# Kernel optimization log

Hardware: AMD Instinct MI355X
Metric: run time of the kernel (lower is better)

The kernel has to match this reference:

```python
import jax, jax.numpy as jnp
import numpy as np

B, M, C = 32, 64, 36
INPUT_DIM, HIDDEN, N_CLASS = 1024, 512, 1000
NEG_INF = -1e10


def setup_inputs() -> dict:
    key = jax.random.key(0)
    ks = jax.random.split(key, 16)
    s = 0.02
    return {
        "mention_embeddings": jax.random.normal(ks[0], (B, M, INPUT_DIM), jnp.float32),
        "class_labels": jax.random.uniform(ks[1], (B, C, N_CLASS), jnp.float32),
        "mention_mask": jnp.ones((B, M), jnp.float32),
        "class_mask": jnp.ones((B, C), jnp.float32),
        # visual_embedder: Linear(n_class, H) -> ReLU -> Linear(H, H)
        "vw1": jax.random.normal(ks[2], (N_CLASS, HIDDEN), jnp.float32) * s,
        "vb1": jnp.zeros((HIDDEN,), jnp.float32),
        "vw2": jax.random.normal(ks[3], (HIDDEN, HIDDEN), jnp.float32) * s,
        "vb2": jnp.zeros((HIDDEN,), jnp.float32),
        # mention_embedder: Linear(input_dim, H) -> ReLU -> Linear(H, H)
        "mw1": jax.random.normal(ks[4], (INPUT_DIM, HIDDEN), jnp.float32) * s,
        "mb1": jnp.zeros((HIDDEN,), jnp.float32),
        "mw2": jax.random.normal(ks[5], (HIDDEN, HIDDEN), jnp.float32) * s,
        "mb2": jnp.zeros((HIDDEN,), jnp.float32),
        # attention: Linear(H, H) -> ReLU -> Linear(H, 1)
        "aw1": jax.random.normal(ks[6], (HIDDEN, HIDDEN), jnp.float32) * s,
        "ab1": jnp.zeros((HIDDEN,), jnp.float32),
        "aw2": jax.random.normal(ks[7], (HIDDEN, 1), jnp.float32) * s,
        "ab2": jnp.zeros((1,), jnp.float32),
    }


def reference(mention_embeddings, class_labels, mention_mask, class_mask,
              vw1, vb1, vw2, vb2, mw1, mb1, mw2, mb2, aw1, ab1, aw2, ab2):
    # visual embeddings: (B, C, H)
    vis = jax.nn.relu(class_labels @ vw1 + vb1) @ vw2 + vb2
    # mention embeddings: (B, M, H)
    men = jax.nn.relu(mention_embeddings @ mw1 + mb1) @ mw2 + mb2
    # broadcast outer product: (B, M, C, H)
    prod = men[:, :, None, :] * vis[:, None, :, :]
    # 2-layer MLP attention score -> (B, M, C)
    h = jax.nn.relu(prod @ aw1 + ab1)
    attn = (h @ aw2 + ab2)[..., 0]
    # masking
    attn = attn * mention_mask[:, :, None] * class_mask[:, None, :]
    attn = jnp.where(attn != 0, attn, NEG_INF)
    return attn
```

## Files before the change

### kernel.cpp

```cpp
#include <hip/hip_runtime.h>

typedef _Float16 f16;
typedef _Float16 f16x8 __attribute__((ext_vector_type(8)));
typedef _Float16 f16x4 __attribute__((ext_vector_type(4)));
typedef float f32x4 __attribute__((ext_vector_type(4)));
typedef float fl4 __attribute__((ext_vector_type(4)));

#define NEG_INF_F (-1e10f)

__device__ __forceinline__ void stage16(const f16* g, f16* l) {
    __builtin_amdgcn_global_load_lds((const __attribute__((address_space(1))) void*)g,
                                     (__attribute__((address_space(3))) void*)l, 16, 0, 0);
}

__global__ __launch_bounds__(256) void prep2(const float* __restrict__ me,
                                             const float* __restrict__ mw1,
                                             const float* __restrict__ vw1,
                                             const float* __restrict__ mw2,
                                             const float* __restrict__ vw2,
                                             const float* __restrict__ aw1,
                                             const float* __restrict__ cl,
                                             f16* __restrict__ me_h,
                                             f16* __restrict__ mw1t, f16* __restrict__ vw1t,
                                             f16* __restrict__ mw2t, f16* __restrict__ vw2t,
                                             f16* __restrict__ aw1t, f16* __restrict__ cl_h) {
    int bx = blockIdx.x, t = threadIdx.x;
    if (bx < 1792) {
        __shared__ float tile[32][33];
        const float* src; f16* dst; int Ksrc, Kp, tid;
        if (bx < 512)       { src = mw1; dst = mw1t; Ksrc = 1024; Kp = 1024; tid = bx; }
        else if (bx < 1024) { src = vw1; dst = vw1t; Ksrc = 1000; Kp = 1024; tid = bx - 512; }
        else if (bx < 1280) { src = mw2; dst = mw2t; Ksrc = 512;  Kp = 512;  tid = bx - 1024; }
        else if (bx < 1536) { src = vw2; dst = vw2t; Ksrc = 512;  Kp = 512;  tid = bx - 1280; }
        else                { src = aw1; dst = aw1t; Ksrc = 512;  Kp = 512;  tid = bx - 1536; }
        int tk = tid >> 4, tn = tid & 15;
        int x = t & 31, y = t >> 5;
        #pragma unroll
        for (int r = 0; r < 4; r++) {
            int k = tk * 32 + y * 4 + r;
            tile[y * 4 + r][x] = (k < Ksrc) ? src[k * 512 + tn * 32 + x] : 0.f;
        }
        __syncthreads();
        #pragma unroll
        for (int r = 0; r < 4; r++) {
            int n = tn * 32 + y * 4 + r;
            dst[n * Kp + tk * 32 + x] = (f16)tile[x][y * 4 + r];
        }
        return;
    }
    if (bx < 3840) {
        int i = (bx - 1792) * 256 + t;
        fl4 v = *(const fl4*)(me + i * 4);
        f16x4 h;
        #pragma unroll
        for (int e = 0; e < 4; e++) h[e] = (f16)v[e];
        *(f16x4*)(me_h + i * 4) = h;
        return;
    }
    {
        int i = (bx - 3840) * 256 + t;
        int idx = i * 4;
        int r = idx >> 10, k0 = idx & 1023;
        f16x4 h;
        if (k0 < 1000) {
            fl4 v = *(const fl4*)(cl + r * 1000 + k0);
            #pragma unroll
            for (int e = 0; e < 4; e++) h[e] = (f16)v[e];
        } else {
            #pragma unroll
            for (int e = 0; e < 4; e++) h[e] = (f16)0.f;
        }
        *(f16x4*)(cl_h + idx) = h;
    }
}

__global__ __launch_bounds__(256, 4) void gemm_stg2(const f16* __restrict__ Am,
                                                    const f16* __restrict__ Av,
                                                    const f16* __restrict__ Wm,
                                                    const f16* __restrict__ Wv,
                                                    const float* __restrict__ bm,
                                                    const float* __restrict__ bv,
                                                    f16* __restrict__ om,
                                                    f16* __restrict__ ov,
                                                    int K, int relu) {
    __shared__ f16 ab[2][2048], bb[2][2048];

    int t = threadIdx.x, lane = t & 63, w = t >> 6;
    int rl = lane & 15, kg = lane >> 4;
    int mq = w & 1, nq = w >> 1;
    bool isv = blockIdx.x >= 32;
    int mb = isv ? blockIdx.x - 32 : blockIdx.x;
    const f16* A = isv ? Av : Am;
    const f16* Wt = isv ? Wv : Wm;
    const float* bias = isv ? bv : bm;
    f16* out = isv ? ov : om;
    int m0 = mb * 64, n0 = blockIdx.y * 64;
    int pu = kg ^ ((rl >> 1) & 3);

    int srow = t >> 2;
    int sk8 = (t & 3) ^ ((srow >> 1) & 3);
    const f16* a_src = A + (m0 + srow) * K + sk8 * 8;
    const f16* b_src = Wt + (n0 + srow) * K + sk8 * 8;
    int nsteps = K >> 5;

    f32x4 acc[2][2] = {};

    stage16(a_src, &ab[0][t * 8]);
    stage16(b_src, &bb[0][t * 8]);
    __syncthreads();

    for (int s = 0; s < nsteps; s++) {
        int cur = s & 1;
        if (s + 1 < nsteps) {
            int k1 = (s + 1) * 32;
            stage16(a_src + k1, &ab[cur ^ 1][t * 8]);
            stage16(b_src + k1, &bb[cur ^ 1][t * 8]);
        }
        f16x8 af[2], bf[2];
        #pragma unroll
        for (int f = 0; f < 2; f++) {
            af[f] = *(const f16x8*)&ab[cur][((mq * 32 + f * 16 + rl) * 4 + pu) * 8];
            bf[f] = *(const f16x8*)&bb[cur][((nq * 32 + f * 16 + rl) * 4 + pu) * 8];
        }
        #pragma unroll
        for (int fi = 0; fi < 2; fi++)
            #pragma unroll
            for (int fj = 0; fj < 2; fj++)
                acc[fi][fj] = __builtin_amdgcn_mfma_f32_16x16x32_f16(af[fi], bf[fj], acc[fi][fj], 0, 0, 0);
        __syncthreads();
    }

    #pragma unroll
    for (int fi = 0; fi < 2; fi++)
        #pragma unroll
        for (int fj = 0; fj < 2; fj++) {
            int col = n0 + nq * 32 + fj * 16 + rl;
            float bv2 = bias[col];
            #pragma unroll
            for (int r = 0; r < 4; r++) {
                int row = m0 + mq * 32 + fi * 16 + kg * 4 + r;
                float v = acc[fi][fj][r] + bv2;
                if (relu) v = fmaxf(v, 0.f);
                out[row * 512 + col] = (f16)v;
            }
        }
}

__global__ __launch_bounds__(512, 3) void attn_f12(const f16* __restrict__ men,
                                                   const f16* __restrict__ vis,
                                                   const f16* __restrict__ aw1t,
                                                   const float* __restrict__ ab1,
                                                   const float* __restrict__ aw2,
                                                   float* __restrict__ partial) {
    __shared__ f16 awb[3][4096];
    __shared__ f16 mnb[3][2048];
    __shared__ f16 vist[2048];
    __shared__ float red[2][4][64];

    int t = threadIdx.x, lane = t & 63, w = t >> 6;
    int ms = w & 3, jq = w >> 2;
    int cq = blockIdx.x, jh = blockIdx.y, b = blockIdx.z;
    int c0 = cq * 4;
    int rl = lane & 15, kg = lane >> 4;
    int pu = kg ^ ((rl >> 1) & 3);
    bool w4 = (w < 4);

    int srow = t >> 2;
    int sk8 = (t & 3) ^ ((srow >> 1) & 3);
    const f16* aw_src = aw1t + (jh * 128 + srow) * 512 + sk8 * 8;
    const f16* mn_src = men + (b * 64 + srow) * 512 + sk8 * 8;
    const f16* vi_src = vis + (b * 36 + c0 + (t >> 6)) * 512 + (t & 63) * 8;

    f32x4 acc[4][4] = {};

    if (w4) stage16(vi_src, &vist[t * 8]);
    stage16(aw_src, &awb[0][t * 8]);
    if (w4) stage16(mn_src, &mnb[0][t * 8]);
    stage16(aw_src + 32, &awb[1][t * 8]);
    if (w4) stage16(mn_src + 32, &mnb[1][t * 8]);
    if (w4) asm volatile("s_waitcnt vmcnt(2)" ::: "memory");
    else    asm volatile("s_waitcnt vmcnt(1)" ::: "memory");
    __builtin_amdgcn_s_barrier();
    __builtin_amdgcn_sched_barrier(0);

    #pragma unroll
    for (int s = 0; s < 16; s++) {
        if (s > 0) {
            if (s == 15)  asm volatile("s_waitcnt vmcnt(0)" ::: "memory");
            else if (w4)  asm volatile("s_waitcnt vmcnt(2)" ::: "memory");
            else          asm volatile("s_waitcnt vmcnt(1)" ::: "memory");
            __builtin_amdgcn_s_barrier();
            __builtin_amdgcn_sched_barrier(0);
        }
        if (s <= 13) {
            int k2 = (s + 2) * 32;
            stage16(aw_src + k2, &awb[(s + 2) % 3][t * 8]);
            if (w4) stage16(mn_src + k2, &mnb[(s + 2) % 3][t * 8]);
        }

        const int cur = s % 3;
        f16x8 mm, bf[4], vv[4];
        mm = *(const f16x8*)&mnb[cur][((ms * 16 + rl) * 4 + pu) * 8];
        #pragma unroll
        for (int fj = 0; fj < 4; fj++)
            bf[fj] = *(const f16x8*)&awb[cur][((jq * 64 + fj * 16 + rl) * 4 + pu) * 8];
        #pragma unroll
        for (int c = 0; c < 4; c++)
            vv[c] = *(const f16x8*)&vist[c * 512 + s * 32 + kg * 8];

        #pragma unroll
        for (int c = 0; c < 4; c++) {
            f16x8 a = mm * vv[c];
            #pragma unroll
            for (int fj = 0; fj < 4; fj++)
                acc[c][fj] = __builtin_amdgcn_mfma_f32_16x16x32_f16(a, bf[fj], acc[c][fj], 0, 0, 0);
        }
    }

    int j0 = jh * 128 + jq * 64;
    float ab1v[4], aw2v[4];
    #pragma unroll
    for (int fj = 0; fj < 4; fj++) {
        int j = j0 + fj * 16 + rl;
        ab1v[fj] = ab1[j];
        aw2v[fj] = aw2[j];
    }
    #pragma unroll
    for (int c = 0; c < 4; c++) {
        float part[4];
        #pragma unroll
        for (int r = 0; r < 4; r++) {
            float sv = 0.f;
            #pragma unroll
            for (int fj = 0; fj < 4; fj++)
                sv += fmaxf(acc[c][fj][r] + ab1v[fj], 0.f) * aw2v[fj];
            part[r] = sv;
        }
        #pragma unroll
        for (int mask = 1; mask < 16; mask <<= 1)
            #pragma unroll
            for (int r = 0; r < 4; r++)
                part[r] += __shfl_xor(part[r], mask);
        float myv = 0.f;
        #pragma unroll
        for (int r = 0; r < 4; r++)
            myv = (rl == r) ? part[r] : myv;
        if (rl < 4) {
            int m = ms * 16 + kg * 4 + rl;
            red[jq][c][m] = myv;
        }
    }
    __syncthreads();

    if (t < 256) {
        int ci = t >> 6, m = t & 63;
        float s = red[0][ci][m] + red[1][ci][m];
        partial[((jh * 32 + b) * 64 + m) * 36 + c0 + ci] = s;
    }
}

__global__ __launch_bounds__(256) void postproc(const float* __restrict__ partial,
                                                const float* __restrict__ mm,
                                                const float* __restrict__ cm,
                                                const float* __restrict__ ab2,
                                                float* __restrict__ out) {
    int i = blockIdx.x * 256 + threadIdx.x;
    int b = i / 2304;
    int rest = i - b * 2304;
    int m = rest / 36, c = rest - m * 36;
    float s = 0.f;
    #pragma unroll
    for (int jh = 0; jh < 4; jh++)
        s += partial[((jh * 32 + b) * 64 + m) * 36 + c];
    float v = (s + ab2[0]) * mm[b * 64 + m] * cm[b * 36 + c];
    out[i] = (v != 0.f) ? v : NEG_INF_F;
}

extern "C" void kernel_launch(void* const* d_in, const int* in_sizes, int n_in,
                              void* d_out, int out_size, void* d_ws, size_t ws_size,
                              hipStream_t stream) {
    const float* ME  = (const float*)d_in[0];
    const float* CL  = (const float*)d_in[1];
    const float* MM  = (const float*)d_in[2];
    const float* CM  = (const float*)d_in[3];
    const float* VW1 = (const float*)d_in[4];
    const float* VB1 = (const float*)d_in[5];
    const float* VW2 = (const float*)d_in[6];
    const float* VB2 = (const float*)d_in[7];
    const float* MW1 = (const float*)d_in[8];
    const float* MB1 = (const float*)d_in[9];
    const float* MW2 = (const float*)d_in[10];
    const float* MB2 = (const float*)d_in[11];
    const float* AW1 = (const float*)d_in[12];
    const float* AB1 = (const float*)d_in[13];
    const float* AW2 = (const float*)d_in[14];
    const float* AB2 = (const float*)d_in[15];
    float* out = (float*)d_out;

    char* ws = (char*)d_ws;
    f16* me_h  = (f16*)ws; ws += (size_t)2048 * 1024 * 2;
    f16* cl_h  = (f16*)ws; ws += (size_t)1152 * 1024 * 2;
    f16* mw1t  = (f16*)ws; ws += (size_t)512 * 1024 * 2;
    f16* vw1t  = (f16*)ws; ws += (size_t)512 * 1024 * 2;
    f16* mw2t  = (f16*)ws; ws += (size_t)512 * 512 * 2;
    f16* vw2t  = (f16*)ws; ws += (size_t)512 * 512 * 2;
    f16* aw1t  = (f16*)ws; ws += (size_t)512 * 512 * 2;
    f16* men1  = (f16*)ws; ws += (size_t)2048 * 512 * 2;
    f16* menh  = (f16*)ws; ws += (size_t)2048 * 512 * 2;
    f16* vis1  = (f16*)ws; ws += (size_t)1152 * 512 * 2;
    f16* vish  = (f16*)ws; ws += (size_t)1152 * 512 * 2;
    float* part = (float*)ws; ws += (size_t)4 * 32 * 64 * 36 * 4;

    prep2<<<4992, 256, 0, stream>>>(ME, MW1, VW1, MW2, VW2, AW1, CL,
                                    me_h, mw1t, vw1t, mw2t, vw2t, aw1t, cl_h);
    gemm_stg2<<<dim3(50, 8), 256, 0, stream>>>(me_h, cl_h, mw1t, vw1t, MB1, VB1,
                                               men1, vis1, 1024, 1);
    gemm_stg2<<<dim3(50, 8), 256, 0, stream>>>(men1, vis1, mw2t, vw2t, MB2, VB2,
                                               menh, vish, 512, 0);
    attn_f12<<<dim3(9, 4, 32), 512, 0, stream>>>(menh, vish, aw1t, AB1, AW2, part);
    postproc<<<288, 256, 0, stream>>>(part, MM, CM, AB2, out);
}
```

Measured before the change: 77.17 us.

## Enlarge per-wave attention tile to 32 rows and halve GEMM barriers

```diff
diff --git a/kernel.cpp b/kernel.cpp
--- a/kernel.cpp
+++ b/kernel.cpp
@@ -74,7 +74,7 @@
     }
 }
 
-__global__ __launch_bounds__(256, 4) void gemm_stg2(const f16* __restrict__ Am,
+__global__ __launch_bounds__(256, 4) void gemm_stg3(const f16* __restrict__ Am,
                                                     const f16* __restrict__ Av,
                                                     const f16* __restrict__ Wm,
                                                     const f16* __restrict__ Wv,
@@ -83,7 +83,7 @@
                                                     f16* __restrict__ om,
                                                     f16* __restrict__ ov,
                                                     int K, int relu) {
-    __shared__ f16 ab[2][2048], bb[2][2048];
+    __shared__ f16 ab[4][2048], bb[4][2048];
 
     int t = threadIdx.x, lane = t & 63, w = t >> 6;
     int rl = lane & 15, kg = lane >> 4;
@@ -101,32 +101,39 @@
     int sk8 = (t & 3) ^ ((srow >> 1) & 3);
     const f16* a_src = A + (m0 + srow) * K + sk8 * 8;
     const f16* b_src = Wt + (n0 + srow) * K + sk8 * 8;
-    int nsteps = K >> 5;
+    int ndbl = K >> 6;
 
     f32x4 acc[2][2] = {};
 
     stage16(a_src, &ab[0][t * 8]);
     stage16(b_src, &bb[0][t * 8]);
+    stage16(a_src + 32, &ab[1][t * 8]);
+    stage16(b_src + 32, &bb[1][t * 8]);
     __syncthreads();
 
-    for (int s = 0; s < nsteps; s++) {
-        int cur = s & 1;
-        if (s + 1 < nsteps) {
-            int k1 = (s + 1) * 32;
-            stage16(a_src + k1, &ab[cur ^ 1][t * 8]);
-            stage16(b_src + k1, &bb[cur ^ 1][t * 8]);
-        }
-        f16x8 af[2], bf[2];
-        #pragma unroll
-        for (int f = 0; f < 2; f++) {
-            af[f] = *(const f16x8*)&ab[cur][((mq * 32 + f * 16 + rl) * 4 + pu) * 8];
-            bf[f] = *(const f16x8*)&bb[cur][((nq * 32 + f * 16 + rl) * 4 + pu) * 8];
-        }
-        #pragma unroll
-        for (int fi = 0; fi < 2; fi++)
-            #pragma unroll
-            for (int fj = 0; fj < 2; fj++)
-                acc[fi][fj] = __builtin_amdgcn_mfma_f32_16x16x32_f16(af[fi], bf[fj], acc[fi][fj], 0, 0, 0);
+    for (int ss = 0; ss < ndbl; ss++) {
+        if (ss + 1 < ndbl) {
+            int ka = (ss * 2 + 2) * 32, kb = (ss * 2 + 3) * 32;
+            stage16(a_src + ka, &ab[(ss * 2 + 2) & 3][t * 8]);
+            stage16(b_src + ka, &bb[(ss * 2 + 2) & 3][t * 8]);
+            stage16(a_src + kb, &ab[(ss * 2 + 3) & 3][t * 8]);
+            stage16(b_src + kb, &bb[(ss * 2 + 3) & 3][t * 8]);
+        }
+        #pragma unroll
+        for (int h = 0; h < 2; h++) {
+            int cur = (ss * 2 + h) & 3;
+            f16x8 af[2], bf[2];
+            #pragma unroll
+            for (int f = 0; f < 2; f++) {
+                af[f] = *(const f16x8*)&ab[cur][((mq * 32 + f * 16 + rl) * 4 + pu) * 8];
+                bf[f] = *(const f16x8*)&bb[cur][((nq * 32 + f * 16 + rl) * 4 + pu) * 8];
+            }
+            #pragma unroll
+            for (int fi = 0; fi < 2; fi++)
+                #pragma unroll
+                for (int fj = 0; fj < 2; fj++)
+                    acc[fi][fj] = __builtin_amdgcn_mfma_f32_16x16x32_f16(af[fi], bf[fj], acc[fi][fj], 0, 0, 0);
+        }
         __syncthreads();
     }
 
@@ -146,7 +153,7 @@
         }
 }
 
-__global__ __launch_bounds__(512, 3) void attn_f12(const f16* __restrict__ men,
+__global__ __launch_bounds__(256, 2) void attn_f14(const f16* __restrict__ men,
                                                    const f16* __restrict__ vis,
                                                    const f16* __restrict__ aw1t,
                                                    const float* __restrict__ ab1,
@@ -158,12 +165,11 @@
     __shared__ float red[2][4][64];
 
     int t = threadIdx.x, lane = t & 63, w = t >> 6;
-    int ms = w & 3, jq = w >> 2;
+    int mh = w & 1, jq = w >> 1;
     int cq = blockIdx.x, jh = blockIdx.y, b = blockIdx.z;
     int c0 = cq * 4;
     int rl = lane & 15, kg = lane >> 4;
     int pu = kg ^ ((rl >> 1) & 3);
-    bool w4 = (w < 4);
 
     int srow = t >> 2;
     int sk8 = (t & 3) ^ ((srow >> 1) & 3);
@@ -171,36 +177,40 @@
     const f16* mn_src = men + (b * 64 + srow) * 512 + sk8 * 8;
     const f16* vi_src = vis + (b * 36 + c0 + (t >> 6)) * 512 + (t & 63) * 8;
 
-    f32x4 acc[4][4] = {};
-
-    if (w4) stage16(vi_src, &vist[t * 8]);
+    f32x4 acc[4][2][4] = {};
+
+    stage16(vi_src, &vist[t * 8]);
     stage16(aw_src, &awb[0][t * 8]);
-    if (w4) stage16(mn_src, &mnb[0][t * 8]);
+    stage16(aw_src + 64 * 512, &awb[0][2048 + t * 8]);
+    stage16(mn_src, &mnb[0][t * 8]);
     stage16(aw_src + 32, &awb[1][t * 8]);
-    if (w4) stage16(mn_src + 32, &mnb[1][t * 8]);
-    if (w4) asm volatile("s_waitcnt vmcnt(2)" ::: "memory");
-    else    asm volatile("s_waitcnt vmcnt(1)" ::: "memory");
+    stage16(aw_src + 64 * 512 + 32, &awb[1][2048 + t * 8]);
+    stage16(mn_src + 32, &mnb[1][t * 8]);
+    asm volatile("s_waitcnt vmcnt(3)" ::: "memory");
     __builtin_amdgcn_s_barrier();
     __builtin_amdgcn_sched_barrier(0);
 
     #pragma unroll
     for (int s = 0; s < 16; s++) {
         if (s > 0) {
-            if (s == 15)  asm volatile("s_waitcnt vmcnt(0)" ::: "memory");
-            else if (w4)  asm volatile("s_waitcnt vmcnt(2)" ::: "memory");
-            else          asm volatile("s_waitcnt vmcnt(1)" ::: "memory");
+            if (s == 15) asm volatile("s_waitcnt vmcnt(0)" ::: "memory");
+            else         asm volatile("s_waitcnt vmcnt(3)" ::: "memory");
             __builtin_amdgcn_s_barrier();
             __builtin_amdgcn_sched_barrier(0);
         }
         if (s <= 13) {
             int k2 = (s + 2) * 32;
-            stage16(aw_src + k2, &awb[(s + 2) % 3][t * 8]);
-            if (w4) stage16(mn_src + k2, &mnb[(s + 2) % 3][t * 8]);
+            int nb = (s + 2) % 3;
+            stage16(aw_src + k2, &awb[nb][t * 8]);
+            stage16(aw_src + 64 * 512 + k2, &awb[nb][2048 + t * 8]);
+            stage16(mn_src + k2, &mnb[nb][t * 8]);
         }
 
         const int cur = s % 3;
-        f16x8 mm, bf[4], vv[4];
-        mm = *(const f16x8*)&mnb[cur][((ms * 16 + rl) * 4 + pu) * 8];
+        f16x8 mm[2], bf[4], vv[4];
+        #pragma unroll
+        for (int fi = 0; fi < 2; fi++)
+            mm[fi] = *(const f16x8*)&mnb[cur][((mh * 32 + fi * 16 + rl) * 4 + pu) * 8];
         #pragma unroll
         for (int fj = 0; fj < 4; fj++)
             bf[fj] = *(const f16x8*)&awb[cur][((jq * 64 + fj * 16 + rl) * 4 + pu) * 8];
@@ -209,12 +219,14 @@
             vv[c] = *(const f16x8*)&vist[c * 512 + s * 32 + kg * 8];
 
         #pragma unroll
-        for (int c = 0; c < 4; c++) {
-            f16x8 a = mm * vv[c];
-            #pragma unroll
-            for (int fj = 0; fj < 4; fj++)
-                acc[c][fj] = __builtin_amdgcn_mfma_f32_16x16x32_f16(a, bf[fj], acc[c][fj], 0, 0, 0);
-        }
+        for (int fi = 0; fi < 2; fi++)
+            #pragma unroll
+            for (int c = 0; c < 4; c++) {
+                f16x8 a = mm[fi] * vv[c];
+                #pragma unroll
+                for (int fj = 0; fj < 4; fj++)
+                    acc[c][fi][fj] = __builtin_amdgcn_mfma_f32_16x16x32_f16(a, bf[fj], acc[c][fi][fj], 0, 0, 0);
+            }
     }
 
     int j0 = jh * 128 + jq * 64;
@@ -227,26 +239,32 @@
     }
     #pragma unroll
     for (int c = 0; c < 4; c++) {
-        float part[4];
-        #pragma unroll
-        for (int r = 0; r < 4; r++) {
-            float sv = 0.f;
-            #pragma unroll
-            for (int fj = 0; fj < 4; fj++)
-                sv += fmaxf(acc[c][fj][r] + ab1v[fj], 0.f) * aw2v[fj];
-            part[r] = sv;
-        }
+        float part[2][4];
+        #pragma unroll
+        for (int fi = 0; fi < 2; fi++)
+            #pragma unroll
+            for (int r = 0; r < 4; r++) {
+                float sv = 0.f;
+                #pragma unroll
+                for (int fj = 0; fj < 4; fj++)
+                    sv += fmaxf(acc[c][fi][fj][r] + ab1v[fj], 0.f) * aw2v[fj];
+                part[fi][r] = sv;
+            }
         #pragma unroll
         for (int mask = 1; mask < 16; mask <<= 1)
             #pragma unroll
+            for (int fi = 0; fi < 2; fi++)
+                #pragma unroll
+                for (int r = 0; r < 4; r++)
+                    part[fi][r] += __shfl_xor(part[fi][r], mask);
+        float myv = 0.f;
+        #pragma unroll
+        for (int fi = 0; fi < 2; fi++)
+            #pragma unroll
             for (int r = 0; r < 4; r++)
-                part[r] += __shfl_xor(part[r], mask);
-        float myv = 0.f;
-        #pragma unroll
-        for (int r = 0; r < 4; r++)
-            myv = (rl == r) ? part[r] : myv;
-        if (rl < 4) {
-            int m = ms * 16 + kg * 4 + rl;
+                myv = (rl == fi * 4 + r) ? part[fi][r] : myv;
+        if (rl < 8) {
+            int m = mh * 32 + (rl >> 2) * 16 + kg * 4 + (rl & 3);
             red[jq][c][m] = myv;
         }
     }
@@ -313,10 +331,10 @@
 
     prep2<<<4992, 256, 0, stream>>>(ME, MW1, VW1, MW2, VW2, AW1, CL,
                                     me_h, mw1t, vw1t, mw2t, vw2t, aw1t, cl_h);
-    gemm_stg2<<<dim3(50, 8), 256, 0, stream>>>(me_h, cl_h, mw1t, vw1t, MB1, VB1,
+    gemm_stg3<<<dim3(50, 8), 256, 0, stream>>>(me_h, cl_h, mw1t, vw1t, MB1, VB1,
                                                men1, vis1, 1024, 1);
-    gemm_stg2<<<dim3(50, 8), 256, 0, stream>>>(men1, vis1, mw2t, vw2t, MB2, VB2,
+    gemm_stg3<<<dim3(50, 8), 256, 0, stream>>>(men1, vis1, mw2t, vw2t, MB2, VB2,
                                                menh, vish, 512, 0);
-    attn_f12<<<dim3(9, 4, 32), 512, 0, stream>>>(menh, vish, aw1t, AB1, AW2, part);
+    attn_f14<<<dim3(9, 4, 32), 256, 0, stream>>>(menh, vish, aw1t, AB1, AW2, part);
     postproc<<<288, 256, 0, stream>>>(part, MM, CM, AB2, out);
 }
```

Result: no change. 76.02 us, median of 2 (-1.5%).
